# Kernel optimization log

Measured on AMD Instinct MI355X. Metric: run time of the kernel, lower is better.

## Reference

```python
import jax, jax.numpy as jnp
import numpy as np

B, S, D, H = 4, 1024, 512, 8
HD = D // H          # head_dim = 64
WIN = 32
EMB_HID = 128
NEG = -1e10


def _rel_coords_log():
    # __make_pair_wise_relative_positions: 2D meshgrid over window indexes
    idx = jnp.arange(WIN)
    coords = jnp.stack(jnp.meshgrid(idx, idx, indexing='ij'), 0).reshape(2, -1)  # [2, S]
    rel = coords[:, :, None] - coords[:, None, :]                                # [2, S, S]
    rel = rel.transpose(1, 2, 0).reshape(-1, 2).astype(jnp.float32)              # [S*S, 2]
    return jnp.sign(rel) * jnp.log1p(jnp.abs(rel))


def setup_inputs() -> dict:
    key = jax.random.key(0)
    ks = jax.random.split(key, 16)
    sd = 1.0 / np.sqrt(D)
    p = lambda k, sh, s: (jax.random.normal(k, sh, jnp.float32) * s)
    return {
        'query': jax.random.normal(ks[0], (B, S, D), jnp.float32),
        'key':   jax.random.normal(ks[1], (B, S, D), jnp.float32),
        'value': jax.random.normal(ks[2], (B, S, D), jnp.float32),
        'mask':  jnp.ones((B, 1, 1, S), jnp.int64),
        'Wq': p(ks[3], (D, D), sd), 'bq': jnp.zeros((D,), jnp.float32),
        'Wk': p(ks[4], (D, D), sd), 'bk': jnp.zeros((D,), jnp.float32),
        'Wv': p(ks[5], (D, D), sd), 'bv': jnp.zeros((D,), jnp.float32),
        'Wo': p(ks[6], (D, D), sd), 'bo': jnp.zeros((D,), jnp.float32),
        'W1': p(ks[7], (2, EMB_HID), 0.7), 'b1': jnp.zeros((EMB_HID,), jnp.float32),
        'W2': p(ks[8], (EMB_HID, H), 0.1), 'b2': jnp.zeros((H,), jnp.float32),
    }


def reference(query, key, value, mask, Wq, bq, Wk, bk, Wv, bv, Wo, bo, W1, b1, W2, b2):
    scale = jnp.sqrt(jnp.float32(HD))
    Q = (query @ Wq + bq).reshape(B, S, H, HD).transpose(0, 2, 1, 3)  # [B,H,S,HD]
    K = (key   @ Wk + bk).reshape(B, S, H, HD).transpose(0, 2, 1, 3)
    V = (value @ Wv + bv).reshape(B, S, H, HD).transpose(0, 2, 1, 3)

    energy = jnp.einsum('bhqd,bhkd->bhqk', Q, K) / scale             # [B,H,S,S]

    # continuous position bias: MLP(2 -> EMB_HID -> H) on log-spaced rel coords
    rel = _rel_coords_log()                                           # [S*S, 2]
    bias = jax.nn.relu(rel @ W1 + b1) @ W2 + b2                       # [S*S, H]
    bias = bias.T.reshape(H, S, S)[None]                              # [1,H,S,S]
    energy = energy + bias

    energy = jnp.where(mask == 0, NEG, energy)
    attention = jax.nn.softmax(energy, axis=-1)                       # [B,H,S,S]
    x = jnp.einsum('bhqk,bhkd->bhqd', attention, V)                   # dropout p=0
    x = x.transpose(0, 2, 1, 3).reshape(B, S, D)
    x = x @ Wo + bo
    return x, attention
```

## Files before the change

### kernel.cpp

```cpp
#include <hip/hip_runtime.h>
#include <hip/hip_bf16.h>

typedef __attribute__((ext_vector_type(4))) float f32x4;
typedef __attribute__((ext_vector_type(8))) short bf16x8;
typedef __attribute__((ext_vector_type(4))) unsigned short u16x4;

#define DEVI __device__ __forceinline__

constexpr int B_ = 4, S_ = 1024, D_ = 512, H_ = 8, HD_ = 64;
constexpr float CSH = 11.0903548f;

DEVI unsigned short f2b(float f) {
  union { float f; unsigned u; } v; v.f = f;
  unsigned r = v.u + 0x7fffu + ((v.u >> 16) & 1u);
  return (unsigned short)(r >> 16);
}

DEVI float b2f(unsigned short u) {
  union { unsigned u; float f; } v; v.u = ((unsigned)u) << 16;
  return v.f;
}

__global__ __launch_bounds__(256) void k_prep(const float* Wa, const float* Wb,
                                              const float* Wc, const float* Wd,
                                              unsigned short* T0, unsigned short* T1,
                                              unsigned short* T2, unsigned short* T3,
                                              const float* mW1, const float* mb1,
                                              const float* mW2, const float* mb2,
                                              float* table) {
  if (blockIdx.z == 4) {
    if (blockIdx.y != 0) return;
    int idx = blockIdx.x * 256 + threadIdx.x;
    if (idx >= 63 * 63) return;
    int dy = idx / 63 - 31, dx = idx % 63 - 31;
    float r0 = copysignf(log1pf(fabsf((float)dy)), (float)dy);
    float r1 = copysignf(log1pf(fabsf((float)dx)), (float)dx);
    float acc[8];
#pragma unroll
    for (int h = 0; h < 8; ++h) acc[h] = mb2[h];
    for (int j = 0; j < 128; ++j) {
      float hv = fmaxf(r0 * mW1[j] + r1 * mW1[128 + j] + mb1[j], 0.f);
#pragma unroll
      for (int h = 0; h < 8; ++h) acc[h] += hv * mW2[j * 8 + h];
    }
#pragma unroll
    for (int h = 0; h < 8; ++h) table[h * 3969 + idx] = acc[h] - CSH;
    return;
  }
  const float* W = blockIdx.z == 0 ? Wa : blockIdx.z == 1 ? Wb : blockIdx.z == 2 ? Wc : Wd;
  unsigned short* T = blockIdx.z == 0 ? T0 : blockIdx.z == 1 ? T1 : blockIdx.z == 2 ? T2 : T3;
  __shared__ float tile[32][33];
  int tx = threadIdx.x & 31, ty = threadIdx.x >> 5;
  int n0 = blockIdx.x * 32, k0 = blockIdx.y * 32;
#pragma unroll
  for (int r = 0; r < 4; ++r) tile[ty + r * 8][tx] = W[(size_t)(k0 + ty + r * 8) * D_ + n0 + tx];
  __syncthreads();
#pragma unroll
  for (int r = 0; r < 4; ++r) T[(size_t)(n0 + ty + r * 8) * D_ + k0 + tx] = f2b(tile[tx][ty + r * 8]);
}

__global__ __launch_bounds__(256) void k_gemm_qkv(const float* Aq, const float* Ak, const float* Av,
                                                  const unsigned short* Tq, const unsigned short* Tk,
                                                  const unsigned short* Tv,
                                                  const float* bqv, const float* bkv, const float* bvv,
                                                  unsigned short* Oq, unsigned short* Ok,
                                                  unsigned short* OvT) {
  const float* A = blockIdx.z == 0 ? Aq : blockIdx.z == 1 ? Ak : Av;
  const unsigned short* BT = blockIdx.z == 0 ? Tq : blockIdx.z == 1 ? Tk : Tv;
  const float* bias = blockIdx.z == 0 ? bqv : blockIdx.z == 1 ? bkv : bvv;

  __shared__ unsigned short As[64][72];
  __shared__ unsigned short Bs[128][72];
  const int tid = threadIdx.x;
  const int lane = tid & 63, wave = tid >> 6;
  const int lr = lane & 15, lg = lane >> 4;
  const int wm = (wave >> 1) * 32, wn = (wave & 1) * 64;
  const int m0 = blockIdx.x * 64, n0 = blockIdx.y * 128;

  f32x4 acc[2][4];
#pragma unroll
  for (int i = 0; i < 2; ++i)
#pragma unroll
    for (int j = 0; j < 4; ++j) acc[i][j] = (f32x4){0.f, 0.f, 0.f, 0.f};

  for (int k0 = 0; k0 < 512; k0 += 64) {
#pragma unroll
    for (int i = 0; i < 4; ++i) {
      int idx = tid + i * 256;
      int r = idx >> 4, c4 = (idx & 15) * 4;
      float4 fv = *(const float4*)(A + (size_t)(m0 + r) * 512 + k0 + c4);
      u16x4 wv;
      wv[0] = f2b(fv.x); wv[1] = f2b(fv.y); wv[2] = f2b(fv.z); wv[3] = f2b(fv.w);
      *(u16x4*)&As[r][c4] = wv;
    }
#pragma unroll
    for (int i = 0; i < 8; ++i) {
      int idx = tid + i * 256;
      int r = idx >> 4, c4 = (idx & 15) * 4;
      *(u16x4*)&Bs[r][c4] = *(const u16x4*)(BT + (size_t)(n0 + r) * 512 + k0 + c4);
    }
    __syncthreads();
#pragma unroll
    for (int kk = 0; kk < 2; ++kk) {
      bf16x8 af[2], bg[4];
#pragma unroll
      for (int i = 0; i < 2; ++i) af[i] = *(const bf16x8*)&As[wm + i * 16 + lr][kk * 32 + lg * 8];
#pragma unroll
      for (int j = 0; j < 4; ++j) bg[j] = *(const bf16x8*)&Bs[wn + j * 16 + lr][kk * 32 + lg * 8];
#pragma unroll
      for (int i = 0; i < 2; ++i)
#pragma unroll
        for (int j = 0; j < 4; ++j)
          acc[i][j] = __builtin_amdgcn_mfma_f32_16x16x32_bf16(af[i], bg[j], acc[i][j], 0, 0, 0);
    }
    __syncthreads();
  }

#pragma unroll
  for (int i = 0; i < 2; ++i)
#pragma unroll
    for (int j = 0; j < 4; ++j) {
      int mbase = m0 + wm + i * 16 + lg * 4;
      int n = n0 + wn + j * 16 + lr;
      float bvl = bias[n];
      int h = n >> 6, hd = n & 63;
      int bseg = mbase >> 10, s0 = mbase & 1023;
      if (blockIdx.z == 2) {
        u16x4 pk;
#pragma unroll
        for (int r = 0; r < 4; ++r) pk[r] = f2b(acc[i][j][r] + bvl);
        *(u16x4*)(OvT + (((size_t)(bseg * H_ + h) * 64 + hd) * 1024 + s0)) = pk;
      } else {
        unsigned short* outp = blockIdx.z == 0 ? Oq : Ok;
#pragma unroll
        for (int r = 0; r < 4; ++r) {
          float v = acc[i][j][r] + bvl;
          outp[(((size_t)bseg * H_ + h) * S_ + s0 + r) * HD_ + hd] = f2b(v);
        }
      }
    }
}

__global__ __launch_bounds__(256) void k_gemm_out(const unsigned short* A, const unsigned short* BT,
                                                  const float* bias, float* outp) {
  __shared__ unsigned short As[64][72];
  __shared__ unsigned short Bs[128][72];
  const int tid = threadIdx.x;
  const int lane = tid & 63, wave = tid >> 6;
  const int lr = lane & 15, lg = lane >> 4;
  const int wm = (wave >> 1) * 32, wn = (wave & 1) * 64;
  const int m0 = blockIdx.x * 64, n0 = blockIdx.y * 128;

  f32x4 acc[2][4];
#pragma unroll
  for (int i = 0; i < 2; ++i)
#pragma unroll
    for (int j = 0; j < 4; ++j) acc[i][j] = (f32x4){0.f, 0.f, 0.f, 0.f};

  for (int k0 = 0; k0 < 512; k0 += 64) {
#pragma unroll
    for (int i = 0; i < 4; ++i) {
      int idx = tid + i * 256;
      int r = idx >> 4, c4 = (idx & 15) * 4;
      *(u16x4*)&As[r][c4] = *(const u16x4*)(A + (size_t)(m0 + r) * 512 + k0 + c4);
    }
#pragma unroll
    for (int i = 0; i < 8; ++i) {
      int idx = tid + i * 256;
      int r = idx >> 4, c4 = (idx & 15) * 4;
      *(u16x4*)&Bs[r][c4] = *(const u16x4*)(BT + (size_t)(n0 + r) * 512 + k0 + c4);
    }
    __syncthreads();
#pragma unroll
    for (int kk = 0; kk < 2; ++kk) {
      bf16x8 af[2], bg[4];
#pragma unroll
      for (int i = 0; i < 2; ++i) af[i] = *(const bf16x8*)&As[wm + i * 16 + lr][kk * 32 + lg * 8];
#pragma unroll
      for (int j = 0; j < 4; ++j) bg[j] = *(const bf16x8*)&Bs[wn + j * 16 + lr][kk * 32 + lg * 8];
#pragma unroll
      for (int i = 0; i < 2; ++i)
#pragma unroll
        for (int j = 0; j < 4; ++j)
          acc[i][j] = __builtin_amdgcn_mfma_f32_16x16x32_bf16(af[i], bg[j], acc[i][j], 0, 0, 0);
    }
    __syncthreads();
  }

#pragma unroll
  for (int i = 0; i < 2; ++i)
#pragma unroll
    for (int j = 0; j < 4; ++j) {
      int mbase = m0 + wm + i * 16 + lg * 4;
      int n = n0 + wn + j * 16 + lr;
      float bvl = bias[n];
#pragma unroll
      for (int r = 0; r < 4; ++r)
        outp[(size_t)(mbase + r) * 512 + n] = acc[i][j][r] + bvl;
    }
}

__global__ __launch_bounds__(256, 3) void k_attn(const unsigned short* Qb, const unsigned short* Kb,
                                                 const unsigned short* VT, const float* tbl,
                                                 const int* mask, float* out_attn,
                                                 unsigned short* Xp) {
  const int tid = threadIdx.x;
  const int lane = tid & 63, w = tid >> 6;
  const int lr = lane & 15, lg = lane >> 4;
  const int bh = blockIdx.y, b = bh >> 3, h = bh & 7;
  const int q0 = blockIdx.x * 16;

  __shared__ unsigned short Pb[16][1024];
  __shared__ float biasS[2016];
  __shared__ float mbig[1024];
  __shared__ float lsbuf[4][16];
  __shared__ int tbad[16];

  const unsigned short* Qh = Qb + (size_t)bh * (S_ * HD_);
  const unsigned short* Kh = Kb + (size_t)bh * (S_ * HD_);
  const unsigned short* Vth = VT + (size_t)bh * (HD_ * S_);

  if (tid < 16) tbad[tid] = 0;
  __syncthreads();
  {
    const float* tsl = tbl + h * 3969 + (q0 >> 5) * 63;
    for (int i = tid; i < 2016; i += 256) biasS[i] = tsl[i];
  }
  {
    int4 mv = *(const int4*)(mask + b * S_ + tid * 4);
    int base = tid * 4;
    mbig[base] = mv.x ? 3.0e38f : -30.f;
    mbig[base + 1] = mv.y ? 3.0e38f : -30.f;
    mbig[base + 2] = mv.z ? 3.0e38f : -30.f;
    mbig[base + 3] = mv.w ? 3.0e38f : -30.f;
    if (!(mv.x && mv.y && mv.z && mv.w)) tbad[base >> 6] = 1;
  }

  const int qrow = q0 + lr;
  const bf16x8 bq0 = *(const bf16x8*)(Qh + (size_t)qrow * 64 + lg * 8);
  const bf16x8 bq1 = *(const bf16x8*)(Qh + (size_t)qrow * 64 + 32 + lg * 8);
  const int qj31 = (q0 & 31) + lr + 31;

  float ls = 0.f;
  __syncthreads();

#pragma unroll
  for (int it = 0; it < 4; ++it) {
    const int gt = w * 4 + it;
    const bool bad = tbad[gt] != 0;
#pragma unroll
    for (int fn = 0; fn < 4; ++fn) {
      const unsigned short* kb = Kh + (size_t)(gt * 64 + fn * 16 + lr) * 64 + lg * 8;
      bf16x8 a0 = *(const bf16x8*)(kb);
      bf16x8 a1 = *(const bf16x8*)(kb + 32);
      f32x4 s = (f32x4){0.f, 0.f, 0.f, 0.f};
      s = __builtin_amdgcn_mfma_f32_16x16x32_bf16(a0, bq0, s, 0, 0, 0);
      s = __builtin_amdgcn_mfma_f32_16x16x32_bf16(a1, bq1, s, 0, 0, 0);
      u16x4 pb;
#pragma unroll
      for (int r = 0; r < 4; ++r) {
        int bidx = (31 - gt * 2 - (fn >> 1)) * 63 + qj31 - (fn & 1) * 16 - lg * 4 - r;
        float arg = fmaf(s[r], 0.125f, biasS[bidx]);
        if (bad) arg = fminf(arg, mbig[gt * 64 + fn * 16 + lg * 4 + r]);
        float p = __expf(arg);
        ls += p;
        pb[r] = f2b(p);
      }
      int s8 = (gt * 16 + fn * 4 + lg) ^ ((lr & 7) << 1);
      *(u16x4*)((char*)&Pb[lr][0] + s8 * 8) = pb;
    }
  }
  ls += __shfl_xor(ls, 16, 64);
  ls += __shfl_xor(ls, 32, 64);
  if (lg == 0) lsbuf[w][lr] = ls;
  __syncthreads();

  const float inv = 1.f / (lsbuf[0][lr] + lsbuf[1][lr] + lsbuf[2][lr] + lsbuf[3][lr]);

  f32x4 invs;
#pragma unroll
  for (int j = 0; j < 4; ++j) invs[j] = __shfl(inv, j * 4 + lg, 64);
  float* oa = out_attn + (size_t)bh * (S_ * S_) + (size_t)q0 * S_ + w * 256;
#pragma unroll
  for (int i = 0; i < 16; ++i) {
    int qv = (i & 3) * 4 + lg;
    int kk = (i >> 2) * 64 + lr * 4;
    int s8 = ((w * 256 + kk) >> 2) ^ ((qv & 7) << 1);
    u16x4 pb = *(const u16x4*)((const char*)&Pb[qv][0] + s8 * 8);
    f32x4 pr;
#pragma unroll
    for (int r = 0; r < 4; ++r) pr[r] = b2f(pb[r]) * invs[i & 3];
    *(f32x4*)(oa + (size_t)qv * S_ + kk) = pr;
  }

  f32x4 of = (f32x4){0.f, 0.f, 0.f, 0.f};
  const unsigned short* vb = Vth + (size_t)(w * 16 + lr) * 1024 + lg * 8;
#pragma unroll
  for (int gt = 0; gt < 16; ++gt) {
#pragma unroll
    for (int sub = 0; sub < 2; ++sub) {
      int c16 = (gt * 8 + sub * 4 + lg) ^ (lr & 7);
      bf16x8 pa = *(const bf16x8*)((const char*)&Pb[lr][0] + c16 * 16);
      bf16x8 bv = *(const bf16x8*)(vb + gt * 64 + sub * 32);
      of = __builtin_amdgcn_mfma_f32_16x16x32_bf16(pa, bv, of, 0, 0, 0);
    }
  }

  f32x4 invq;
#pragma unroll
  for (int r = 0; r < 4; ++r) invq[r] = __shfl(inv, lg * 4 + r, 64);
#pragma unroll
  for (int r = 0; r < 4; ++r) {
    int q = q0 + lg * 4 + r;
    Xp[((size_t)b * S_ + q) * D_ + h * 64 + w * 16 + lr] = f2b(of[r] * invq[r]);
  }
}

extern "C" void kernel_launch(void* const* d_in, const int* in_sizes, int n_in,
                              void* d_out, int out_size, void* d_ws, size_t ws_size,
                              hipStream_t stream) {
  const float* query = (const float*)d_in[0];
  const float* key   = (const float*)d_in[1];
  const float* value = (const float*)d_in[2];
  const int*   maskp = (const int*)d_in[3];
  const float* Wq = (const float*)d_in[4];
  const float* bq = (const float*)d_in[5];
  const float* Wk = (const float*)d_in[6];
  const float* bk = (const float*)d_in[7];
  const float* Wv = (const float*)d_in[8];
  const float* bv = (const float*)d_in[9];
  const float* Wo = (const float*)d_in[10];
  const float* bo = (const float*)d_in[11];
  const float* W1 = (const float*)d_in[12];
  const float* b1 = (const float*)d_in[13];
  const float* W2 = (const float*)d_in[14];
  const float* b2 = (const float*)d_in[15];

  char* ws = (char*)d_ws;
  const size_t MB4 = (size_t)4 * 1024 * 1024;
  unsigned short* Qb  = (unsigned short*)(ws);
  unsigned short* Kb  = (unsigned short*)(ws + MB4);
  unsigned short* VT  = (unsigned short*)(ws + 2 * MB4);
  unsigned short* Xp  = (unsigned short*)(ws + 3 * MB4);
  unsigned short* WqT = (unsigned short*)(ws + 4 * MB4);
  unsigned short* WkT = (unsigned short*)(ws + 4 * MB4 + 524288);
  unsigned short* WvT = (unsigned short*)(ws + 4 * MB4 + 2 * 524288);
  unsigned short* WoT = (unsigned short*)(ws + 4 * MB4 + 3 * 524288);
  float* table        = (float*)(ws + 4 * MB4 + 4 * 524288);

  float* out_x = (float*)d_out;
  float* out_attn = out_x + (size_t)B_ * S_ * D_;

  k_prep<<<dim3(16, 16, 5), 256, 0, stream>>>(Wq, Wk, Wv, Wo, WqT, WkT, WvT, WoT,
                                              W1, b1, W2, b2, table);
  k_gemm_qkv<<<dim3(64, 4, 3), 256, 0, stream>>>(query, key, value, WqT, WkT, WvT,
                                                 bq, bk, bv, Qb, Kb, VT);
  k_attn<<<dim3(64, 32), 256, 0, stream>>>(Qb, Kb, VT, table, maskp, out_attn, Xp);
  k_gemm_out<<<dim3(64, 4), 256, 0, stream>>>(Xp, WoT, bo, out_x);
}
```

Baseline: 120.9 us.

## Retile attention to 32 query rows per block with split-K PV fused into score loop

Each attention block now handles 32 query rows instead of 16, with warps split into two query halves and two key halves. Each warp accumulates P·V partial sums inside the score loop, so loaded K/V tiles are reused across more queries. The two key-half partials are combined through shared memory, where a union buffer aliases the bias, mask and output scratch. The grid is flattened with a head-major ordering to improve L2 locality, and the attention-probability store is rewritten so each lane writes contiguous 64-byte row segments. The doubled P buffer raises LDS use and lowers occupancy from 3 to 2 blocks per CU.

```diff
diff --git a/kernel.cpp b/kernel.cpp
--- a/kernel.cpp
+++ b/kernel.cpp
@@ -200,21 +200,29 @@
     }
 }
 
-__global__ __launch_bounds__(256, 3) void k_attn(const unsigned short* Qb, const unsigned short* Kb,
+__global__ __launch_bounds__(256, 2) void k_attn(const unsigned short* Qb, const unsigned short* Kb,
                                                  const unsigned short* VT, const float* tbl,
                                                  const int* mask, float* out_attn,
                                                  unsigned short* Xp) {
   const int tid = threadIdx.x;
   const int lane = tid & 63, w = tid >> 6;
   const int lr = lane & 15, lg = lane >> 4;
-  const int bh = blockIdx.y, b = bh >> 3, h = bh & 7;
-  const int q0 = blockIdx.x * 16;
-
-  __shared__ unsigned short Pb[16][1024];
-  __shared__ float biasS[2016];
-  __shared__ float mbig[1024];
+  const int wq = w & 1, wk = w >> 1;
+
+  const int flat = blockIdx.x;
+  const int bh = (flat & 7) + 8 * (flat >> 8);
+  const int qt = (flat >> 3) & 31;
+  const int b = bh >> 3, h = bh & 7;
+  const int q0 = qt * 32;
+
+  __shared__ unsigned short Pb[32][1024];
+  __shared__ __align__(16) char uni[12160];
   __shared__ float lsbuf[4][16];
   __shared__ int tbad[16];
+
+  float* biasS = (float*)uni;
+  float* mbig = (float*)(uni + 8064);
+  float* Obuf = (float*)uni;
 
   const unsigned short* Qh = Qb + (size_t)bh * (S_ * HD_);
   const unsigned short* Kh = Kb + (size_t)bh * (S_ * HD_);
@@ -236,83 +244,107 @@
     if (!(mv.x && mv.y && mv.z && mv.w)) tbad[base >> 6] = 1;
   }
 
-  const int qrow = q0 + lr;
+  const int qloc = wq * 16 + lr;
+  const int qrow = q0 + qloc;
   const bf16x8 bq0 = *(const bf16x8*)(Qh + (size_t)qrow * 64 + lg * 8);
   const bf16x8 bq1 = *(const bf16x8*)(Qh + (size_t)qrow * 64 + 32 + lg * 8);
-  const int qj31 = (q0 & 31) + lr + 31;
-
+  const int qj31 = qloc + 31;
+  const int pm = (qloc & 7) << 1;
+
+  f32x4 of[4];
+#pragma unroll
+  for (int i = 0; i < 4; ++i) of[i] = (f32x4){0.f, 0.f, 0.f, 0.f};
   float ls = 0.f;
   __syncthreads();
 
 #pragma unroll
-  for (int it = 0; it < 4; ++it) {
-    const int gt = w * 4 + it;
+  for (int it = 0; it < 8; ++it) {
+    const int gt = wk * 8 + it;
     const bool bad = tbad[gt] != 0;
+    const unsigned short* ktb = Kh + (size_t)gt * 64 * 64;
 #pragma unroll
     for (int fn = 0; fn < 4; ++fn) {
-      const unsigned short* kb = Kh + (size_t)(gt * 64 + fn * 16 + lr) * 64 + lg * 8;
+      const unsigned short* kb = ktb + (fn * 16 + lr) * 64 + lg * 8;
       bf16x8 a0 = *(const bf16x8*)(kb);
       bf16x8 a1 = *(const bf16x8*)(kb + 32);
       f32x4 s = (f32x4){0.f, 0.f, 0.f, 0.f};
       s = __builtin_amdgcn_mfma_f32_16x16x32_bf16(a0, bq0, s, 0, 0, 0);
       s = __builtin_amdgcn_mfma_f32_16x16x32_bf16(a1, bq1, s, 0, 0, 0);
+      const int ib = (31 - gt * 2 - (fn >> 1)) * 63 + qj31 - (fn & 1) * 16 - lg * 4;
       u16x4 pb;
 #pragma unroll
       for (int r = 0; r < 4; ++r) {
-        int bidx = (31 - gt * 2 - (fn >> 1)) * 63 + qj31 - (fn & 1) * 16 - lg * 4 - r;
-        float arg = fmaf(s[r], 0.125f, biasS[bidx]);
+        float arg = fmaf(s[r], 0.125f, biasS[ib - r]);
         if (bad) arg = fminf(arg, mbig[gt * 64 + fn * 16 + lg * 4 + r]);
         float p = __expf(arg);
         ls += p;
         pb[r] = f2b(p);
       }
-      int s8 = (gt * 16 + fn * 4 + lg) ^ ((lr & 7) << 1);
-      *(u16x4*)((char*)&Pb[lr][0] + s8 * 8) = pb;
-    }
-  }
+      int s8 = (gt * 16 + fn * 4 + lg) ^ pm;
+      *(u16x4*)((char*)&Pb[qloc][0] + s8 * 8) = pb;
+    }
+#pragma unroll
+    for (int c = 0; c < 2; ++c) {
+      int s8 = (gt * 16 + c * 8 + lg * 2) ^ pm;
+      bf16x8 pa = *(const bf16x8*)((const char*)&Pb[qloc][0] + s8 * 8);
+#pragma unroll
+      for (int fn2 = 0; fn2 < 4; ++fn2) {
+        bf16x8 bv = *(const bf16x8*)(Vth + (size_t)(fn2 * 16 + lr) * 1024 + gt * 64 + c * 32 + lg * 8);
+        of[fn2] = __builtin_amdgcn_mfma_f32_16x16x32_bf16(pa, bv, of[fn2], 0, 0, 0);
+      }
+    }
+  }
+
   ls += __shfl_xor(ls, 16, 64);
   ls += __shfl_xor(ls, 32, 64);
   if (lg == 0) lsbuf[w][lr] = ls;
   __syncthreads();
 
-  const float inv = 1.f / (lsbuf[0][lr] + lsbuf[1][lr] + lsbuf[2][lr] + lsbuf[3][lr]);
-
-  f32x4 invs;
-#pragma unroll
-  for (int j = 0; j < 4; ++j) invs[j] = __shfl(inv, j * 4 + lg, 64);
-  float* oa = out_attn + (size_t)bh * (S_ * S_) + (size_t)q0 * S_ + w * 256;
-#pragma unroll
-  for (int i = 0; i < 16; ++i) {
-    int qv = (i & 3) * 4 + lg;
-    int kk = (i >> 2) * 64 + lr * 4;
-    int s8 = ((w * 256 + kk) >> 2) ^ ((qv & 7) << 1);
-    u16x4 pb = *(const u16x4*)((const char*)&Pb[qv][0] + s8 * 8);
-    f32x4 pr;
-#pragma unroll
-    for (int r = 0; r < 4; ++r) pr[r] = b2f(pb[r]) * invs[i & 3];
-    *(f32x4*)(oa + (size_t)qv * S_ + kk) = pr;
-  }
-
-  f32x4 of = (f32x4){0.f, 0.f, 0.f, 0.f};
-  const unsigned short* vb = Vth + (size_t)(w * 16 + lr) * 1024 + lg * 8;
-#pragma unroll
-  for (int gt = 0; gt < 16; ++gt) {
-#pragma unroll
-    for (int sub = 0; sub < 2; ++sub) {
-      int c16 = (gt * 8 + sub * 4 + lg) ^ (lr & 7);
-      bf16x8 pa = *(const bf16x8*)((const char*)&Pb[lr][0] + c16 * 16);
-      bf16x8 bv = *(const bf16x8*)(vb + gt * 64 + sub * 32);
-      of = __builtin_amdgcn_mfma_f32_16x16x32_bf16(pa, bv, of, 0, 0, 0);
-    }
-  }
-
-  f32x4 invq;
-#pragma unroll
-  for (int r = 0; r < 4; ++r) invq[r] = __shfl(inv, lg * 4 + r, 64);
-#pragma unroll
-  for (int r = 0; r < 4; ++r) {
-    int q = q0 + lg * 4 + r;
-    Xp[((size_t)b * S_ + q) * D_ + h * 64 + w * 16 + lr] = f2b(of[r] * invq[r]);
+  const float inv = 1.f / (lsbuf[wq][lr] + lsbuf[wq + 2][lr]);
+
+  if (wk == 1) {
+#pragma unroll
+    for (int fn2 = 0; fn2 < 4; ++fn2)
+#pragma unroll
+      for (int r = 0; r < 4; ++r)
+        Obuf[(wq * 16 + lg * 4 + r) * 68 + fn2 * 16 + lr] = of[fn2][r];
+  }
+  __syncthreads();
+  if (wk == 0) {
+    f32x4 invq;
+#pragma unroll
+    for (int r = 0; r < 4; ++r) invq[r] = __shfl(inv, lg * 4 + r, 64);
+#pragma unroll
+    for (int fn2 = 0; fn2 < 4; ++fn2)
+#pragma unroll
+      for (int r = 0; r < 4; ++r) {
+        int q = q0 + wq * 16 + lg * 4 + r;
+        float val = (of[fn2][r] + Obuf[(wq * 16 + lg * 4 + r) * 68 + fn2 * 16 + lr]) * invq[r];
+        Xp[((size_t)b * S_ + q) * D_ + h * 64 + fn2 * 16 + lr] = f2b(val);
+      }
+  }
+
+  float* oa = out_attn + (size_t)bh * (S_ * S_) + (size_t)qrow * S_;
+#pragma unroll
+  for (int step = 0; step < 8; ++step) {
+    const int kbase = wk * 512 + step * 64 + lg * 16;
+    const int k4 = kbase >> 2;
+    u16x4 p0 = *(const u16x4*)((const char*)&Pb[qloc][0] + ((k4 ^ pm) * 8));
+    u16x4 p1 = *(const u16x4*)((const char*)&Pb[qloc][0] + (((k4 + 1) ^ pm) * 8));
+    u16x4 p2 = *(const u16x4*)((const char*)&Pb[qloc][0] + (((k4 + 2) ^ pm) * 8));
+    u16x4 p3 = *(const u16x4*)((const char*)&Pb[qloc][0] + (((k4 + 3) ^ pm) * 8));
+    f32x4 o0, o1, o2, o3;
+#pragma unroll
+    for (int r = 0; r < 4; ++r) {
+      o0[r] = b2f(p0[r]) * inv;
+      o1[r] = b2f(p1[r]) * inv;
+      o2[r] = b2f(p2[r]) * inv;
+      o3[r] = b2f(p3[r]) * inv;
+    }
+    *(f32x4*)(oa + kbase) = o0;
+    *(f32x4*)(oa + kbase + 4) = o1;
+    *(f32x4*)(oa + kbase + 8) = o2;
+    *(f32x4*)(oa + kbase + 12) = o3;
   }
 }
 
@@ -355,6 +387,6 @@
                                               W1, b1, W2, b2, table);
   k_gemm_qkv<<<dim3(64, 4, 3), 256, 0, stream>>>(query, key, value, WqT, WkT, WvT,
                                                  bq, bk, bv, Qb, Kb, VT);
-  k_attn<<<dim3(64, 32), 256, 0, stream>>>(Qb, Kb, VT, table, maskp, out_attn, Xp);
+  k_attn<<<dim3(1024), 256, 0, stream>>>(Qb, Kb, VT, table, maskp, out_attn, Xp);
   k_gemm_out<<<dim3(64, 4), 256, 0, stream>>>(Xp, WoT, bo, out_x);
 }
```

Result: slower. 150.4 us (+24.4%).
